# Performance work log

Measured on AMD Instinct MI355X. Metric: run time of the kernel, lower is better.

Reference implementation:

```python
import jax, jax.numpy as jnp
import numpy as np


def setup_inputs() -> dict:
    key = jax.random.key(0)
    k1, k2 = jax.random.split(key)
    N, I, J, K = 256, 32, 32, 256
    x = jax.random.normal(k1, (N, I, K), dtype=jnp.float32)
    z = jax.random.normal(k2, (N, J, K), dtype=jnp.float32)
    return {"x": x, "z": z}


def reference(x, z):
    # Original torch code loops over batch rolls; rolling only permutes the set
    # over which log_softmax (a permutation-invariant logsumexp) is taken, and
    # index 0 of the roll stack is always the diagonal pair (x[n], z[n]).
    # So it is exactly a symmetric InfoNCE over the full pairwise score matrix.
    J = z.shape[1]
    # Full pairwise token-level similarity: [N_x, N_z, I, J]
    sim = jnp.einsum('aik,bjk->abij', x, z)
    # score(x_a, z_b) = sum_{i,j} softmax_i(sim)*sim / J
    w = jax.nn.softmax(sim, axis=2) * sim
    S = w.sum(axis=(2, 3)) / J  # [N_x, N_z]
    diag = jnp.diagonal(S)
    # loss_x[n] = -log_softmax over x-candidates (axis 0) at the diagonal
    loss_x = jax.nn.logsumexp(S, axis=0) - diag
    # loss_z[n] = -log_softmax over z-candidates (axis 1) at the diagonal
    loss_z = jax.nn.logsumexp(S, axis=1) - diag
    loss = loss_x + loss_z
    return loss.mean()  # reduction='mean'
```

## Files before the change

kernel.cpp:

```cpp
#include <hip/hip_runtime.h>
#include <hip/hip_bf16.h>
#include <hip/hip_fp16.h>
#include <stdint.h>


typedef __attribute__((ext_vector_type(8))) short short8;
typedef __attribute__((ext_vector_type(16))) float float16;
typedef __attribute__((ext_vector_type(8))) int int8v;
typedef __attribute__((ext_vector_type(4))) int int4v;

typedef const __attribute__((address_space(1))) unsigned int* gptr_as1;
typedef __attribute__((address_space(3))) unsigned int* lptr_as3;

#define NTOK 256
#define KDIM 256

__device__ __forceinline__ unsigned short f2bf(float f) {
    unsigned int u = __float_as_uint(f);
    unsigned int r = (u + 0x7fffu + ((u >> 16) & 1u)) >> 16;
    return (unsigned short)r;
}

__device__ __forceinline__ short8 cvt8(const float* p) {
    float4 f0 = ((const float4*)p)[0];
    float4 f1 = ((const float4*)p)[1];
    short8 v;
    v[0] = (short)f2bf(f0.x); v[1] = (short)f2bf(f0.y);
    v[2] = (short)f2bf(f0.z); v[3] = (short)f2bf(f0.w);
    v[4] = (short)f2bf(f1.x); v[5] = (short)f2bf(f1.y);
    v[6] = (short)f2bf(f1.z); v[7] = (short)f2bf(f1.w);
    return v;
}

__global__ void conv_fp8(const float* __restrict__ x,
                         const float* __restrict__ z,
                         int4v* __restrict__ q,
                         float* __restrict__ out0) {
    const int uid = blockIdx.x * 256 + threadIdx.x;
    if (uid == 0) out0[0] = 0.0f;
    const int tensor = uid >> 16;
    const int idx    = uid & 65535;
    const int g    = idx >> 8;
    const int r    = idx & 255;
    const int ks   = r >> 6;
    const int lane = r & 63;
    const int row  = g * 32 + (lane & 31);
    const int k0   = ks * 64 + (lane >> 5) * 32;
    const float4* p = (const float4*)((tensor ? z : x) + row * KDIM + k0);

    int4v lo, hi;
#pragma unroll
    for (int i = 0; i < 4; i++) {
        float4 f = p[i];
        int v = __builtin_amdgcn_cvt_pk_fp8_f32(f.x, f.y, 0, false);
        v = __builtin_amdgcn_cvt_pk_fp8_f32(f.z, f.w, v, true);
        lo[i] = v;
    }
#pragma unroll
    for (int i = 0; i < 4; i++) {
        float4 f = p[4 + i];
        int v = __builtin_amdgcn_cvt_pk_fp8_f32(f.x, f.y, 0, false);
        v = __builtin_amdgcn_cvt_pk_fp8_f32(f.z, f.w, v, true);
        hi[i] = v;
    }
    q[tensor * 131072 + idx]         = lo;
    q[tensor * 131072 + 65536 + idx] = hi;
}

__device__ __forceinline__ int8v mk8(int4v lo, int4v hi) {
    int8v r;
    r[0] = lo[0]; r[1] = lo[1]; r[2] = lo[2]; r[3] = lo[3];
    r[4] = hi[0]; r[5] = hi[1]; r[6] = hi[2]; r[7] = hi[3];
    return r;
}

#define MFMA_FP8(a, b, c) \
    __builtin_amdgcn_mfma_scale_f32_32x32x64_f8f6f4((a), (b), (c), 0, 0, 0, 0x7F7F7F7F, 0, 0x7F7F7F7F)

__device__ __forceinline__ void tile_epilogue_sp(const float16& c, __half* __restrict__ Sp,
                                                 int a, int b, int lane) {
    float m8[8], m4[4];
#pragma unroll
    for (int r = 0; r < 8; r++) m8[r] = fmaxf(c[2 * r], c[2 * r + 1]);
#pragma unroll
    for (int r = 0; r < 4; r++) m4[r] = fmaxf(m8[2 * r], m8[2 * r + 1]);
    float m = fmaxf(fmaxf(m4[0], m4[1]), fmaxf(m4[2], m4[3]));
    m = fmaxf(m, __shfl_xor(m, 32, 64));

    float s0 = 0.f, s1 = 0.f, s2 = 0.f, s3 = 0.f;
    float w0 = 0.f, w1 = 0.f, w2 = 0.f, w3 = 0.f;
#pragma unroll
    for (int r = 0; r < 16; r += 4) {
        float e0 = __expf(c[r + 0] - m);
        float e1 = __expf(c[r + 1] - m);
        float e2 = __expf(c[r + 2] - m);
        float e3 = __expf(c[r + 3] - m);
        s0 += e0; s1 += e1; s2 += e2; s3 += e3;
        w0 = fmaf(e0, c[r + 0], w0);
        w1 = fmaf(e1, c[r + 1], w1);
        w2 = fmaf(e2, c[r + 2], w2);
        w3 = fmaf(e3, c[r + 3], w3);
    }
    float se  = (s0 + s1) + (s2 + s3);
    float swe = (w0 + w1) + (w2 + w3);
    se  += __shfl_xor(se, 32, 64);
    swe += __shfl_xor(swe, 32, 64);
    float cv = swe * __builtin_amdgcn_rcpf(se);
    Sp[(((a << 8) + b) << 6) + lane] = __float2half_rn(cv);
}

__global__ __launch_bounds__(256, 2)
void sim_fp8(const int4v* __restrict__ q, __half* __restrict__ Sp) {
    __shared__ int4v sA[2048];

    const int tid  = threadIdx.x;
    const int lane = tid & 63;
    const int w    = tid >> 6;

    const int ablk = blockIdx.x >> 5;
    const int bblk = blockIdx.x & 31;
    const int ag0  = ablk * 4;
    const int bg0  = bblk * 8 + w * 2;

#pragma unroll
    for (int i = 0; i < 8; i++) {
        const int chunk = i * 4 + w;
        const int ai = chunk >> 3;
        const int ks = (chunk >> 1) & 3;
        const int h  = chunk & 1;
        const int4v* g = q + h * 65536 + ((ag0 + ai) * 4 + ks) * 64 + lane;
        int4v* l = &sA[chunk * 64];
        __builtin_amdgcn_global_load_lds((gptr_as1)g, (lptr_as3)l, 16, 0, 0);
    }
    __syncthreads();

    const int4v* zq = q + 131072;

    float16 acc[4][2];
#pragma unroll
    for (int ai = 0; ai < 4; ai++)
#pragma unroll
        for (int bi = 0; bi < 2; bi++)
#pragma unroll
            for (int r = 0; r < 16; r++) acc[ai][bi][r] = 0.0f;

#pragma unroll
    for (int ks = 0; ks < 4; ks++) {
        const int u0 = ((bg0 + 0) * 4 + ks) * 64 + lane;
        const int u1 = ((bg0 + 1) * 4 + ks) * 64 + lane;
        int8v Ba = mk8(zq[u0], zq[65536 + u0]);
        int8v Bb = mk8(zq[u1], zq[65536 + u1]);
#pragma unroll
        for (int ai = 0; ai < 4; ai++) {
            const int base = (ai * 8 + ks * 2) * 64 + lane;
            int8v Af = mk8(sA[base], sA[base + 64]);
            acc[ai][0] = MFMA_FP8(Af, Ba, acc[ai][0]);
            acc[ai][1] = MFMA_FP8(Af, Bb, acc[ai][1]);
        }
    }

#pragma unroll
    for (int ai = 0; ai < 4; ai++)
#pragma unroll
        for (int bi = 0; bi < 2; bi++)
            tile_epilogue_sp(acc[ai][bi], Sp, ag0 + ai, bg0 + bi, lane);
}

__global__ void conv_kernel(const float* __restrict__ x,
                            const float* __restrict__ z,
                            short8* __restrict__ outbf,
                            float* __restrict__ out0) {
    const int uid = blockIdx.x * 256 + threadIdx.x;
    if (uid == 0) out0[0] = 0.0f;
    const int u = uid & 262143;
    const float* src = (uid < 262144) ? x : z;
    const int g  = u >> 10;
    const int r  = u & 1023;
    const int ks = r >> 6;
    const int h  = (r >> 5) & 1;
    const int l  = r & 31;
    outbf[uid] = cvt8(src + ((g * 32 + l) * KDIM + ks * 16 + h * 8));
}

__device__ __forceinline__ void tile_epilogue_bf(const float16& c, float* __restrict__ S,
                                                 int a, int b, int lane) {
    float m8[8], m4[4];
#pragma unroll
    for (int r = 0; r < 8; r++) m8[r] = fmaxf(c[2 * r], c[2 * r + 1]);
#pragma unroll
    for (int r = 0; r < 4; r++) m4[r] = fmaxf(m8[2 * r], m8[2 * r + 1]);
    float m = fmaxf(fmaxf(m4[0], m4[1]), fmaxf(m4[2], m4[3]));
    m = fmaxf(m, __shfl_xor(m, 32, 64));

    float s0 = 0.f, s1 = 0.f, s2 = 0.f, s3 = 0.f;
    float w0 = 0.f, w1 = 0.f, w2 = 0.f, w3 = 0.f;
#pragma unroll
    for (int r = 0; r < 16; r += 4) {
        float e0 = __expf(c[r + 0] - m);
        float e1 = __expf(c[r + 1] - m);
        float e2 = __expf(c[r + 2] - m);
        float e3 = __expf(c[r + 3] - m);
        s0 += e0; s1 += e1; s2 += e2; s3 += e3;
        w0 = fmaf(e0, c[r + 0], w0);
        w1 = fmaf(e1, c[r + 1], w1);
        w2 = fmaf(e2, c[r + 2], w2);
        w3 = fmaf(e3, c[r + 3], w3);
    }
    float se  = (s0 + s1) + (s2 + s3);
    float swe = (w0 + w1) + (w2 + w3);
    se  += __shfl_xor(se, 32, 64);
    swe += __shfl_xor(swe, 32, 64);
    float cv = swe * __builtin_amdgcn_rcpf(se);
#pragma unroll
    for (int off = 1; off < 32; off <<= 1) cv += __shfl_xor(cv, off, 64);
    if (lane == 0) S[a * NTOK + b] = cv * (1.0f / 32.0f);
}

#define MFMA_BF16 __builtin_amdgcn_mfma_f32_32x32x16_bf16

template <bool F32SRC>
__global__ __launch_bounds__(256, 2)
void sim_kernel(const short8* __restrict__ xbf, const short8* __restrict__ zbf,
                const float* __restrict__ xf, const float* __restrict__ zf,
                float* __restrict__ S) {
    __shared__ short8 sA[4096];

    const int tid  = threadIdx.x;
    const int lane = tid & 63;
    const int w    = tid >> 6;
    const int l31  = lane & 31;
    const int half = lane >> 5;

    const int ablk = blockIdx.x >> 5;
    const int bblk = blockIdx.x & 31;
    const int ag0  = ablk * 4;
    const int bg0  = bblk * 8 + w * 2;

    float16 acc[4][2];
#pragma unroll
    for (int ai = 0; ai < 4; ai++)
#pragma unroll
        for (int bi = 0; bi < 2; bi++)
#pragma unroll
            for (int r = 0; r < 16; r++) acc[ai][bi][r] = 0.0f;

    if (!F32SRC) {
        const short8* asrc = xbf + (size_t)ablk * 4096;
#pragma unroll
        for (int i = 0; i < 16; i++) {
            const short8* g = asrc + i * 256 + w * 64 + lane;
            short8* l = &sA[i * 256 + w * 64];
            __builtin_amdgcn_global_load_lds((gptr_as1)g, (lptr_as3)l, 16, 0, 0);
        }
        __syncthreads();

        const short8* pb0 = zbf + (bg0 + 0) * 1024 + lane;
        const short8* pb1 = zbf + (bg0 + 1) * 1024 + lane;
        short8 Ba = pb0[0];
        short8 Bb = pb1[0];
#pragma unroll
        for (int ks = 0; ks < 16; ks++) {
            short8 Na, Nb;
            if (ks < 15) { Na = pb0[(ks + 1) * 64]; Nb = pb1[(ks + 1) * 64]; }
            short8 A0 = sA[ks * 64 + lane];
            short8 A1 = sA[1024 + ks * 64 + lane];
            short8 A2 = sA[2048 + ks * 64 + lane];
            short8 A3 = sA[3072 + ks * 64 + lane];
            acc[0][0] = MFMA_BF16(A0, Ba, acc[0][0], 0, 0, 0);
            acc[0][1] = MFMA_BF16(A0, Bb, acc[0][1], 0, 0, 0);
            acc[1][0] = MFMA_BF16(A1, Ba, acc[1][0], 0, 0, 0);
            acc[1][1] = MFMA_BF16(A1, Bb, acc[1][1], 0, 0, 0);
            acc[2][0] = MFMA_BF16(A2, Ba, acc[2][0], 0, 0, 0);
            acc[2][1] = MFMA_BF16(A2, Bb, acc[2][1], 0, 0, 0);
            acc[3][0] = MFMA_BF16(A3, Ba, acc[3][0], 0, 0, 0);
            acc[3][1] = MFMA_BF16(A3, Bb, acc[3][1], 0, 0, 0);
            Ba = Na; Bb = Nb;
        }
    } else {
        const float* fb0 = zf + (((bg0 + 0) * 32 + l31) * KDIM + half * 8);
        const float* fb1 = zf + (((bg0 + 1) * 32 + l31) * KDIM + half * 8);
#pragma unroll 1
        for (int ks = 0; ks < 16; ks++) {
            short8 Ba = cvt8(fb0 + ks * 16);
            short8 Bb = cvt8(fb1 + ks * 16);
#pragma unroll
            for (int ai = 0; ai < 4; ai++) {
                const float* fa = xf + (((ag0 + ai) * 32 + l31) * KDIM + half * 8);
                short8 Af = cvt8(fa + ks * 16);
                acc[ai][0] = MFMA_BF16(Af, Ba, acc[ai][0], 0, 0, 0);
                acc[ai][1] = MFMA_BF16(Af, Bb, acc[ai][1], 0, 0, 0);
            }
        }
    }

#pragma unroll
    for (int ai = 0; ai < 4; ai++)
#pragma unroll
        for (int bi = 0; bi < 2; bi++)
            tile_epilogue_bf(acc[ai][bi], S, ag0 + ai, bg0 + bi, lane);
}

__global__ void red_kernel(const __half* __restrict__ Sp, float* __restrict__ S) {
    const int t = blockIdx.x * 256 + threadIdx.x;
    const __half2* h2 = (const __half2*)(Sp + (size_t)t * 64);
    float s = 0.0f;
#pragma unroll
    for (int i = 0; i < 32; i++) {
        float2 f = __half22float2(h2[i]);
        s += f.x + f.y;
    }
    S[t] = s * (1.0f / 64.0f);
}

__global__ void loss_part(const float* __restrict__ S, float* __restrict__ out) {
    const int lane = threadIdx.x & 63;
    const int wid  = threadIdx.x >> 6;
    const int n    = blockIdx.x * 4 + wid;

    float cv[4], rv[4];
#pragma unroll
    for (int k = 0; k < 4; k++) {
        const int t = lane + 64 * k;
        cv[k] = S[t * NTOK + n];
        rv[k] = S[n * NTOK + t];
    }
    float m = fmaxf(fmaxf(cv[0], cv[1]), fmaxf(cv[2], cv[3]));
#pragma unroll
    for (int off = 1; off < 64; off <<= 1) m = fmaxf(m, __shfl_xor(m, off, 64));
    float s = 0.0f;
#pragma unroll
    for (int k = 0; k < 4; k++) s += __expf(cv[k] - m);
#pragma unroll
    for (int off = 1; off < 64; off <<= 1) s += __shfl_xor(s, off, 64);
    float lse_col = m + __logf(s);

    float m2 = fmaxf(fmaxf(rv[0], rv[1]), fmaxf(rv[2], rv[3]));
#pragma unroll
    for (int off = 1; off < 64; off <<= 1) m2 = fmaxf(m2, __shfl_xor(m2, off, 64));
    float s2 = 0.0f;
#pragma unroll
    for (int k = 0; k < 4; k++) s2 += __expf(rv[k] - m2);
#pragma unroll
    for (int off = 1; off < 64; off <<= 1) s2 += __shfl_xor(s2, off, 64);
    float lse_row = m2 + __logf(s2);

    __shared__ float red[4];
    if (lane == 0) {
        float diag = S[n * NTOK + n];
        red[wid] = (lse_col - diag) + (lse_row - diag);
    }
    __syncthreads();
    if (threadIdx.x == 0)
        atomicAdd(out, (red[0] + red[1] + red[2] + red[3]) * (1.0f / 256.0f));
}

__global__ void zero_kernel(float* __restrict__ out) {
    out[0] = 0.0f;
}

extern "C" void kernel_launch(void* const* d_in, const int* in_sizes, int n_in,
                              void* d_out, int out_size, void* d_ws, size_t ws_size,
                              hipStream_t stream) {
    const float* x = (const float*)d_in[0];
    const float* z = (const float*)d_in[1];
    float* out = (float*)d_out;

    const size_t q_bytes  = 262144ull * 16ull;
    const size_t sp_bytes = 65536ull * 64ull * 2ull;
    const size_t s_bytes  = 256ull * 256ull * 4ull;
    const size_t bf_bytes = 524288ull * 16ull;

    if (ws_size >= q_bytes + sp_bytes + s_bytes) {
        int4v*  q  = (int4v*)d_ws;
        __half* Sp = (__half*)((char*)d_ws + q_bytes);
        float*  S  = (float*)((char*)d_ws + q_bytes + sp_bytes);
        conv_fp8<<<512, 256, 0, stream>>>(x, z, q, out);
        sim_fp8<<<2048, 256, 0, stream>>>(q, Sp);
        red_kernel<<<256, 256, 0, stream>>>(Sp, S);
        loss_part<<<64, 256, 0, stream>>>(S, out);
    } else if (ws_size >= bf_bytes + s_bytes) {
        short8* xbf = (short8*)d_ws;
        short8* zbf = xbf + 262144;
        float*  S   = (float*)((char*)d_ws + bf_bytes);
        conv_kernel<<<2048, 256, 0, stream>>>(x, z, (short8*)d_ws, out);
        sim_kernel<false><<<2048, 256, 0, stream>>>(xbf, zbf, nullptr, nullptr, S);
        loss_part<<<64, 256, 0, stream>>>(S, out);
    } else {
        float* S = (float*)d_ws;
        zero_kernel<<<1, 1, 0, stream>>>(out);
        sim_kernel<true><<<2048, 256, 0, stream>>>(nullptr, nullptr, x, z, S);
        loss_part<<<64, 256, 0, stream>>>(S, out);
    }
}
```

Before: 97.16 us.

## Fuse partial-score reduction into loss kernel and halve partial-score writes

The fp8 similarity epilogue now writes only 32 half-precision partials per pair (lanes 0-31, which already hold the xor-32 reduced value) instead of 64 duplicates. The separate reduction kernel is dropped; a new loss kernel reads the partials for one row and one column per block, sums them, and computes both logsumexps and the diagonal term directly. This removes one kernel launch, the S round trip, and half the Sp traffic. In exchange each partial is read twice (once as a row, once as a column), and the column reads are strided.

After: 96.33 us. Within noise of the previous version (-0.8%).

```diff
diff --git a/kernel.cpp b/kernel.cpp
--- a/kernel.cpp
+++ b/kernel.cpp
@@ -106,7 +106,8 @@
     se  += __shfl_xor(se, 32, 64);
     swe += __shfl_xor(swe, 32, 64);
     float cv = swe * __builtin_amdgcn_rcpf(se);
-    Sp[(((a << 8) + b) << 6) + lane] = __float2half_rn(cv);
+    if (lane < 32)
+        Sp[(((a << 8) + b) << 5) + lane] = __float2half_rn(cv);
 }
 
 __global__ __launch_bounds__(256, 2)
@@ -124,12 +125,12 @@
 
 #pragma unroll
     for (int i = 0; i < 8; i++) {
-        const int chunk = i * 4 + w;
-        const int ai = chunk >> 3;
-        const int ks = (chunk >> 1) & 3;
-        const int h  = chunk & 1;
+        const int c  = i * 4 + w;
+        const int ai = c >> 3;
+        const int ks = (c >> 1) & 3;
+        const int h  = c & 1;
         const int4v* g = q + h * 65536 + ((ag0 + ai) * 4 + ks) * 64 + lane;
-        int4v* l = &sA[chunk * 64];
+        int4v* l = &sA[c * 64];
         __builtin_amdgcn_global_load_lds((gptr_as1)g, (lptr_as3)l, 16, 0, 0);
     }
     __syncthreads();
@@ -164,6 +165,61 @@
 #pragma unroll
         for (int bi = 0; bi < 2; bi++)
             tile_epilogue_sp(acc[ai][bi], Sp, ag0 + ai, bg0 + bi, lane);
+}
+
+__global__ void loss_fused(const __half* __restrict__ Sp, float* __restrict__ out) {
+    const int n    = blockIdx.x;
+    const int k    = threadIdx.x;
+    const int lane = k & 63;
+    const int wv   = k >> 6;
+
+    const __half2* rp = (const __half2*)(Sp + ((size_t)(n * 256 + k) << 5));
+    const __half2* cp = (const __half2*)(Sp + ((size_t)(k * 256 + n) << 5));
+    float rs = 0.f, cs = 0.f;
+#pragma unroll
+    for (int i = 0; i < 16; i++) {
+        float2 f = __half22float2(rp[i]);
+        rs += f.x + f.y;
+    }
+#pragma unroll
+    for (int i = 0; i < 16; i++) {
+        float2 f = __half22float2(cp[i]);
+        cs += f.x + f.y;
+    }
+    rs *= (1.0f / 32.0f);
+    cs *= (1.0f / 32.0f);
+
+    __shared__ float shm[8];
+    __shared__ float shs[8];
+    __shared__ float sdiag;
+    if (k == n) sdiag = rs;
+
+    float mr = rs, mc = cs;
+#pragma unroll
+    for (int off = 1; off < 64; off <<= 1) {
+        mr = fmaxf(mr, __shfl_xor(mr, off, 64));
+        mc = fmaxf(mc, __shfl_xor(mc, off, 64));
+    }
+    if (lane == 0) { shm[wv] = mr; shm[4 + wv] = mc; }
+    __syncthreads();
+    mr = fmaxf(fmaxf(shm[0], shm[1]), fmaxf(shm[2], shm[3]));
+    mc = fmaxf(fmaxf(shm[4], shm[5]), fmaxf(shm[6], shm[7]));
+
+    float er = __expf(rs - mr), ec = __expf(cs - mc);
+#pragma unroll
+    for (int off = 1; off < 64; off <<= 1) {
+        er += __shfl_xor(er, off, 64);
+        ec += __shfl_xor(ec, off, 64);
+    }
+    if (lane == 0) { shs[wv] = er; shs[4 + wv] = ec; }
+    __syncthreads();
+    if (k == 0) {
+        float sr = (shs[0] + shs[1]) + (shs[2] + shs[3]);
+        float sc = (shs[4] + shs[5]) + (shs[6] + shs[7]);
+        float lse_row = mr + __logf(sr);
+        float lse_col = mc + __logf(sc);
+        atomicAdd(out, (lse_row + lse_col - 2.0f * sdiag) * (1.0f / 256.0f));
+    }
 }
 
 __global__ void conv_kernel(const float* __restrict__ x,
@@ -300,18 +356,6 @@
             tile_epilogue_bf(acc[ai][bi], S, ag0 + ai, bg0 + bi, lane);
 }
 
-__global__ void red_kernel(const __half* __restrict__ Sp, float* __restrict__ S) {
-    const int t = blockIdx.x * 256 + threadIdx.x;
-    const __half2* h2 = (const __half2*)(Sp + (size_t)t * 64);
-    float s = 0.0f;
-#pragma unroll
-    for (int i = 0; i < 32; i++) {
-        float2 f = __half22float2(h2[i]);
-        s += f.x + f.y;
-    }
-    S[t] = s * (1.0f / 64.0f);
-}
-
 __global__ void loss_part(const float* __restrict__ S, float* __restrict__ out) {
     const int lane = threadIdx.x & 63;
     const int wid  = threadIdx.x >> 6;
@@ -366,18 +410,16 @@
     float* out = (float*)d_out;
 
     const size_t q_bytes  = 262144ull * 16ull;
-    const size_t sp_bytes = 65536ull * 64ull * 2ull;
+    const size_t sp_bytes = 65536ull * 32ull * 2ull;
     const size_t s_bytes  = 256ull * 256ull * 4ull;
     const size_t bf_bytes = 524288ull * 16ull;
 
-    if (ws_size >= q_bytes + sp_bytes + s_bytes) {
+    if (ws_size >= q_bytes + sp_bytes) {
         int4v*  q  = (int4v*)d_ws;
         __half* Sp = (__half*)((char*)d_ws + q_bytes);
-        float*  S  = (float*)((char*)d_ws + q_bytes + sp_bytes);
         conv_fp8<<<512, 256, 0, stream>>>(x, z, q, out);
         sim_fp8<<<2048, 256, 0, stream>>>(q, Sp);
-        red_kernel<<<256, 256, 0, stream>>>(Sp, S);
-        loss_part<<<64, 256, 0, stream>>>(S, out);
+        loss_fused<<<256, 256, 0, stream>>>(Sp, out);
     } else if (ws_size >= bf_bytes + s_bytes) {
         short8* xbf = (short8*)d_ws;
         short8* zbf = xbf + 262144;
```
